# Optimization experiments

Hardware: AMD Instinct MI355X
Metric: run time of the kernel (lower is better)

Reference implementation:

```python
import jax, jax.numpy as jnp
import numpy as np

B, N, F_IN, F_OUT = 64, 4096, 32, 32


def setup_inputs() -> dict:
    key = jax.random.key(0)
    k1, k2, k3, k4 = jax.random.split(key, 4)
    x = jax.random.normal(k1, (B, N, F_IN), dtype=jnp.float32)
    adj = jax.random.uniform(k2, (N, N), dtype=jnp.float32)
    # GraphConvolution parameters (Glorot-ish scale)
    W = jax.random.normal(k3, (F_IN, F_OUT), dtype=jnp.float32) / np.sqrt(F_IN)
    b = jax.random.normal(k4, (F_OUT,), dtype=jnp.float32) * 0.01
    return {"x": x, "adj": adj, "W": W, "b": b}


def reference(x, adj, W, b):
    # Original: adj_ = kron(I_B, adj) -> block-diagonal [B*N, B*N];
    # gconv(x_flat, adj_) = adj_ @ (x_flat @ W) + b, reshaped to [B, N, F_OUT].
    # Block-diagonal structure == independent per-batch graph conv:
    #   out[b] = adj @ (x[b] @ W) + b
    support = jnp.einsum('bnf,fo->bno', x, W)      # [B, N, F_OUT]
    out = jnp.einsum('nm,bmo->bno', adj, support)  # [B, N, F_OUT]
    return out + b
```

## Files before the change

kernel.cpp:

```cpp
#include <hip/hip_runtime.h>
#include <hip/hip_bf16.h>


#define B_SZ 64
#define N_SZ 4096
#define NT 64
#define STG 49152

typedef __attribute__((ext_vector_type(8))) short bf16x8;
typedef __attribute__((ext_vector_type(4))) float f32x4;
typedef __attribute__((ext_vector_type(8))) unsigned short u16x8;

__device__ __forceinline__ unsigned short f2bf(float f) {
  unsigned int u = __float_as_uint(f);
  u += 0x7fffu + ((u >> 16) & 1u);
  return (unsigned short)(u >> 16);
}

__device__ __forceinline__ void support_body(const float* __restrict__ x,
                                             const float* __restrict__ W,
                                             unsigned short* __restrict__ St,
                                             int gid) {
  const int m = gid & (N_SZ - 1);
  const int b = gid >> 12;
  const float4* xr = (const float4*)(x + (size_t)gid * 32);
  float xv[32];
#pragma unroll
  for (int i = 0; i < 8; ++i) {
    float4 v = xr[i];
    xv[4 * i + 0] = v.x; xv[4 * i + 1] = v.y;
    xv[4 * i + 2] = v.z; xv[4 * i + 3] = v.w;
  }
  const size_t obase = ((size_t)b * 32) * (size_t)N_SZ + m;
#pragma unroll
  for (int o = 0; o < 32; ++o) {
    float acc = 0.f;
#pragma unroll
    for (int f = 0; f < 32; ++f) acc = fmaf(xv[f], W[f * 32 + o], acc);
    St[obase + (size_t)o * N_SZ] = f2bf(acc);
  }
}

__device__ __forceinline__ void cvt_body(const float* __restrict__ a,
                                         unsigned short* __restrict__ o,
                                         size_t idx8) {
  const size_t i = idx8 * 8;
  const float4* p = (const float4*)(a + i);
  float4 v0 = p[0], v1 = p[1];
  u16x8 r;
  r[0] = f2bf(v0.x); r[1] = f2bf(v0.y); r[2] = f2bf(v0.z); r[3] = f2bf(v0.w);
  r[4] = f2bf(v1.x); r[5] = f2bf(v1.y); r[6] = f2bf(v1.z); r[7] = f2bf(v1.w);
  *(u16x8*)(o + i) = r;
}

__global__ __launch_bounds__(256) void k_prep(const float* __restrict__ x,
                                              const float* __restrict__ adj,
                                              const float* __restrict__ W,
                                              unsigned short* __restrict__ St,
                                              unsigned short* __restrict__ adjB) {
  const int bid = blockIdx.x;
  const int t = threadIdx.x;
  if (bid < 8192) cvt_body(adj, adjB, (size_t)bid * 256 + t);
  else support_body(x, W, St, (bid - 8192) * 256 + t);
}

__global__ __launch_bounds__(256) void k_support(const float* __restrict__ x,
                                                 const float* __restrict__ W,
                                                 unsigned short* __restrict__ St) {
  support_body(x, W, St, blockIdx.x * 256 + threadIdx.x);
}
__global__ __launch_bounds__(256) void k_cvt(const float* __restrict__ a,
                                             unsigned short* __restrict__ o) {
  cvt_body(a, o, (size_t)blockIdx.x * 256 + threadIdx.x);
}

#define GLOAD16(gp, lp)                                                        \
  __builtin_amdgcn_global_load_lds(                                            \
      (const __attribute__((address_space(1))) void*)(gp),                     \
      (__attribute__((address_space(3))) void*)(lp), 16, 0, 0)
#define PRIO1() __builtin_amdgcn_s_setprio(1)
#define PRIO0() __builtin_amdgcn_s_setprio(0)
#define VMW(N_) asm volatile("s_waitcnt vmcnt(" #N_ ")" ::: "memory")
#define LGKM0() asm volatile("s_waitcnt lgkmcnt(0)" ::: "memory")
#define BARR() asm volatile("s_barrier" ::: "memory")
#define SCHED0() __builtin_amdgcn_sched_barrier(0)

__global__ __launch_bounds__(512, 2) void k_gemm8(const unsigned short* __restrict__ Ab,
                                                  const unsigned short* __restrict__ Bm,
                                                  const float* __restrict__ bias,
                                                  float* __restrict__ out,
                                                  int nbm, int rowoff) {
  __shared__ __attribute__((aligned(16))) char SM[147456];
  const int t = threadIdx.x;
  const int wg = blockIdx.x;
  const int xcd = wg & 7;
  const int c = wg >> 3;
  const int bm0 = (xcd * nbm + (c >> 3)) << 7;
  const int bn0 = (c & 7) << 8;
  const int lane = t & 63;
  const int wid = t >> 6;
  const int wr = wid & 1;
  const int nc = (wid >> 1) & 1;
  const int ks = wid >> 2;

  f32x4 acc[4][8];
#pragma unroll
  for (int i = 0; i < 4; ++i)
#pragma unroll
    for (int j = 0; j < 8; ++j) acc[i][j] = (f32x4){0.f, 0.f, 0.f, 0.f};

  const int srow = t >> 3;
  const int as = t & 7;
  const int swz = (as ^ (srow & 7)) << 4;
  const size_t a_s0 = ((size_t)(bm0 + srow) << 13) + (size_t)swz;
  const size_t b_s0 = ((size_t)(bn0 + srow) << 13) + (size_t)swz;
  const int t16 = t * 16;
  const char* A8 = (const char*)Ab;
  const char* B8 = (const char*)Bm;

#define STAGE(KT_, LOFF_)                                                      \
  do {                                                                         \
    const size_t kb = (size_t)(KT_) << 7;                                      \
    GLOAD16(A8 + a_s0 + kb,           SM + (LOFF_) + t16);                     \
    GLOAD16(A8 + a_s0 + 524288 + kb,  SM + (LOFF_) + 8192 + t16);              \
    GLOAD16(B8 + b_s0 + kb,           SM + (LOFF_) + 16384 + t16);             \
    GLOAD16(B8 + b_s0 + 524288 + kb,  SM + (LOFF_) + 24576 + t16);             \
    GLOAD16(B8 + b_s0 + 1048576 + kb, SM + (LOFF_) + 32768 + t16);             \
    GLOAD16(B8 + b_s0 + 1572864 + kb, SM + (LOFF_) + 40960 + t16);             \
  } while (0)

  const int cbase = (ks * 64 + ((lane >> 4) << 4)) ^ ((lane & 7) << 4);
  int aoff[4], boff[8];
#pragma unroll
  for (int mi = 0; mi < 4; ++mi)
    aoff[mi] = (wr * 64 + mi * 16 + (lane & 15)) * 128 + cbase;
#pragma unroll
  for (int ni = 0; ni < 8; ++ni)
    boff[ni] = 16384 + (nc * 128 + ni * 16 + (lane & 15)) * 128 + cbase;

#define FRAG_MFMA(CUROFF_)                                                     \
  do {                                                                         \
    bf16x8 a[4], b[8];                                                         \
    _Pragma("unroll") for (int mi = 0; mi < 4; ++mi)                           \
        a[mi] = *(const bf16x8*)(SM + (CUROFF_) + aoff[mi]);                   \
    _Pragma("unroll") for (int ni = 0; ni < 8; ++ni)                           \
        b[ni] = *(const bf16x8*)(SM + (CUROFF_) + boff[ni]);                   \
    LGKM0();                                                                   \
    SCHED0();                                                                  \
    BARR();                                                                    \
    PRIO1();                                                                   \
    _Pragma("unroll") for (int mi = 0; mi < 4; ++mi)                           \
        _Pragma("unroll") for (int ni = 0; ni < 8; ++ni)                       \
            acc[mi][ni] = __builtin_amdgcn_mfma_f32_16x16x32_bf16(             \
                a[mi], b[ni], acc[mi][ni], 0, 0, 0);                           \
    PRIO0();                                                                   \
  } while (0)

#define ITER(T_, CUR_, NXT_)                                                   \
  do {                                                                         \
    STAGE((T_) + 2, (NXT_) * STG);                                             \
    VMW(12);                                                                   \
    BARR();                                                                    \
    FRAG_MFMA((CUR_) * STG);                                                   \
  } while (0)

  STAGE(0, 0);
  STAGE(1, STG);

  for (int t0 = 0; t0 < 60; t0 += 3) {
    ITER(t0 + 0, 0, 2);
    ITER(t0 + 1, 1, 0);
    ITER(t0 + 2, 2, 1);
  }
  ITER(60, 0, 2);
  ITER(61, 1, 0);
  VMW(6);
  BARR();
  FRAG_MFMA(2 * STG);
  VMW(0);
  BARR();
  FRAG_MFMA(0 * STG);

  if (ks == 1) {
    char* mb = SM + ((wid & 3) << 15);
#pragma unroll
    for (int mi = 0; mi < 4; ++mi)
#pragma unroll
      for (int ni = 0; ni < 8; ++ni)
        *(f32x4*)(mb + (((mi * 8 + ni) << 6) + lane) * 16) = acc[mi][ni];
  }
  __syncthreads();
  if (ks == 0) {
    char* mb = SM + ((wid & 3) << 15);
#pragma unroll
    for (int mi = 0; mi < 4; ++mi)
#pragma unroll
      for (int ni = 0; ni < 8; ++ni)
        acc[mi][ni] += *(const f32x4*)(mb + (((mi * 8 + ni) << 6) + lane) * 16);
    const float blo = bias[lane & 15];
    const float bhi = bias[(lane & 15) + 16];
#pragma unroll
    for (int mi = 0; mi < 4; ++mi) {
#pragma unroll
      for (int ni = 0; ni < 8; ++ni) {
        const float badd = (ni & 1) ? bhi : blo;
#pragma unroll
        for (int q = 0; q < 4; ++q) {
          const int n = rowoff + bm0 + wr * 64 + mi * 16 + ((lane >> 4) << 2) + q;
          const int cidx = bn0 + nc * 128 + ni * 16 + (lane & 15);
          const int bb = cidx >> 5;
          const int o = cidx & 31;
          out[(((size_t)bb << 12) + n) * 32 + o] = acc[mi][ni][q] + badd;
        }
      }
    }
  }
}

extern "C" void kernel_launch(void* const* d_in, const int* in_sizes, int n_in,
                              void* d_out, int out_size, void* d_ws, size_t ws_size,
                              hipStream_t stream) {
  const float* x = (const float*)d_in[0];
  const float* adj = (const float*)d_in[1];
  const float* W = (const float*)d_in[2];
  const float* bias = (const float*)d_in[3];
  float* out = (float*)d_out;

  const size_t ST_B = (size_t)2048 * 4096 * 2;
  const size_t ADJ_FULL = (size_t)4096 * 4096 * 2;

  unsigned short* St = (unsigned short*)d_ws;

  if (ws_size >= ST_B + ADJ_FULL) {
    unsigned short* adjB = St + (ST_B / 2);
    hipLaunchKernelGGL(k_prep, dim3(9216), dim3(256), 0, stream, x, adj, W, St,
                       adjB);
    hipLaunchKernelGGL(k_gemm8, dim3(256), dim3(512), 0, stream, adjB, St, bias,
                       out, 4, 0);
  } else {
    unsigned short* adjH = St + (ST_B / 2);
    hipLaunchKernelGGL(k_support, dim3((B_SZ * N_SZ) / 256), dim3(256), 0,
                       stream, x, W, St);
    hipLaunchKernelGGL(k_cvt, dim3((2048 * 4096) / 2048), dim3(256), 0, stream,
                       adj, adjH);
    hipLaunchKernelGGL(k_gemm8, dim3(128), dim3(512), 0, stream, adjH, St, bias,
                       out, 2, 0);
    hipLaunchKernelGGL(k_cvt, dim3((2048 * 4096) / 2048), dim3(256), 0, stream,
                       adj + (size_t)2048 * 4096, adjH);
    hipLaunchKernelGGL(k_gemm8, dim3(128), dim3(512), 0, stream, adjH, St, bias,
                       out, 2, 2048);
  }
}
```

Baseline: 96.89 us.

## Interleave global-to-LDS prefetch with MFMA in four sub-phases per k-tile

Restructures the GEMM main loop so each k-tile is split into four phases. Each phase loads two B fragments from LDS, issues part of the next tile's global_load_lds prefetch, then runs eight MFMAs between barriers. This spreads memory issue across the compute instead of issuing all six loads up front with a single wait. It adds several extra s_barriers per tile and disables loop unrolling, which may add synchronisation overhead.

New measurement: 95.96 us. About the same (-1.0%).

```diff
diff --git a/kernel.cpp b/kernel.cpp
--- a/kernel.cpp
+++ b/kernel.cpp
@@ -82,21 +82,21 @@
 #define PRIO0() __builtin_amdgcn_s_setprio(0)
 #define VMW(N_) asm volatile("s_waitcnt vmcnt(" #N_ ")" ::: "memory")
 #define LGKM0() asm volatile("s_waitcnt lgkmcnt(0)" ::: "memory")
-#define BARR() asm volatile("s_barrier" ::: "memory")
+#define BAR() asm volatile("s_barrier" ::: "memory")
 #define SCHED0() __builtin_amdgcn_sched_barrier(0)
 
-__global__ __launch_bounds__(512, 2) void k_gemm8(const unsigned short* __restrict__ Ab,
-                                                  const unsigned short* __restrict__ Bm,
-                                                  const float* __restrict__ bias,
-                                                  float* __restrict__ out,
-                                                  int nbm, int rowoff) {
+__global__ __launch_bounds__(512, 2) void k_gemm8p(const unsigned short* __restrict__ Ab,
+                                                   const unsigned short* __restrict__ Bm,
+                                                   const float* __restrict__ bias,
+                                                   float* __restrict__ out,
+                                                   int nbm, int rowoff) {
   __shared__ __attribute__((aligned(16))) char SM[147456];
   const int t = threadIdx.x;
   const int wg = blockIdx.x;
   const int xcd = wg & 7;
-  const int c = wg >> 3;
-  const int bm0 = (xcd * nbm + (c >> 3)) << 7;
-  const int bn0 = (c & 7) << 8;
+  const int idx = wg >> 3;
+  const int bm0 = (xcd * nbm + (idx >> 3)) << 7;
+  const int bn0 = (idx & 7) << 8;
   const int lane = t & 63;
   const int wid = t >> 6;
   const int wr = wid & 1;
@@ -118,7 +118,16 @@
   const char* A8 = (const char*)Ab;
   const char* B8 = (const char*)Bm;
 
-#define STAGE(KT_, LOFF_)                                                      \
+  const int cbase = (ks * 64 + ((lane >> 4) << 4)) ^ ((lane & 7) << 4);
+  int aoff[4], boff[8];
+#pragma unroll
+  for (int mi = 0; mi < 4; ++mi)
+    aoff[mi] = (wr * 64 + mi * 16 + (lane & 15)) * 128 + cbase;
+#pragma unroll
+  for (int ni = 0; ni < 8; ++ni)
+    boff[ni] = 16384 + (nc * 128 + ni * 16 + (lane & 15)) * 128 + cbase;
+
+#define STAGEALL(KT_, LOFF_)                                                   \
   do {                                                                         \
     const size_t kb = (size_t)(KT_) << 7;                                      \
     GLOAD16(A8 + a_s0 + kb,           SM + (LOFF_) + t16);                     \
@@ -129,57 +138,70 @@
     GLOAD16(B8 + b_s0 + 1572864 + kb, SM + (LOFF_) + 40960 + t16);             \
   } while (0)
 
-  const int cbase = (ks * 64 + ((lane >> 4) << 4)) ^ ((lane & 7) << 4);
-  int aoff[4], boff[8];
-#pragma unroll
-  for (int mi = 0; mi < 4; ++mi)
-    aoff[mi] = (wr * 64 + mi * 16 + (lane & 15)) * 128 + cbase;
-#pragma unroll
-  for (int ni = 0; ni < 8; ++ni)
-    boff[ni] = 16384 + (nc * 128 + ni * 16 + (lane & 15)) * 128 + cbase;
-
-#define FRAG_MFMA(CUROFF_)                                                     \
+#define MFMA2(N0_, N1_)                                                        \
   do {                                                                         \
+    _Pragma("unroll") for (int mi = 0; mi < 4; ++mi) {                         \
+      acc[mi][N0_] = __builtin_amdgcn_mfma_f32_16x16x32_bf16(                  \
+          a[mi], b[N0_], acc[mi][N0_], 0, 0, 0);                               \
+      acc[mi][N1_] = __builtin_amdgcn_mfma_f32_16x16x32_bf16(                  \
+          a[mi], b[N1_], acc[mi][N1_], 0, 0, 0);                               \
+    }                                                                          \
+  } while (0)
+
+#define TILE(T_, CUR_, NXT_, DOST_, VMN_)                                      \
+  do {                                                                         \
+    const char* Lc = SM + (CUR_) * STG;                                        \
+    char* Ln = SM + (NXT_) * STG;                                              \
+    const size_t kb = ((size_t)(T_) + 2) << 7;                                 \
+    (void)Ln; (void)kb;                                                        \
     bf16x8 a[4], b[8];                                                         \
+                                                   \
     _Pragma("unroll") for (int mi = 0; mi < 4; ++mi)                           \
-        a[mi] = *(const bf16x8*)(SM + (CUROFF_) + aoff[mi]);                   \
-    _Pragma("unroll") for (int ni = 0; ni < 8; ++ni)                           \
-        b[ni] = *(const bf16x8*)(SM + (CUROFF_) + boff[ni]);                   \
-    LGKM0();                                                                   \
-    SCHED0();                                                                  \
-    BARR();                                                                    \
-    PRIO1();                                                                   \
-    _Pragma("unroll") for (int mi = 0; mi < 4; ++mi)                           \
-        _Pragma("unroll") for (int ni = 0; ni < 8; ++ni)                       \
-            acc[mi][ni] = __builtin_amdgcn_mfma_f32_16x16x32_bf16(             \
-                a[mi], b[ni], acc[mi][ni], 0, 0, 0);                           \
-    PRIO0();                                                                   \
+        a[mi] = *(const bf16x8*)(Lc + aoff[mi]);                               \
+    b[0] = *(const bf16x8*)(Lc + boff[0]);                                     \
+    b[1] = *(const bf16x8*)(Lc + boff[1]);                                     \
+    if (DOST_) {                                                               \
+      GLOAD16(A8 + a_s0 + kb, Ln + t16);                                       \
+      GLOAD16(A8 + a_s0 + 524288 + kb, Ln + 8192 + t16);                       \
+    }                                                                          \
+    BAR(); LGKM0(); SCHED0(); PRIO1(); MFMA2(0, 1); PRIO0(); BAR();            \
+                                                           \
+    b[2] = *(const bf16x8*)(Lc + boff[2]);                                     \
+    b[3] = *(const bf16x8*)(Lc + boff[3]);                                     \
+    if (DOST_) GLOAD16(B8 + b_s0 + kb, Ln + 16384 + t16);                      \
+    BAR(); LGKM0(); SCHED0(); PRIO1(); MFMA2(2, 3); PRIO0(); BAR();            \
+                                                           \
+    b[4] = *(const bf16x8*)(Lc + boff[4]);                                     \
+    b[5] = *(const bf16x8*)(Lc + boff[5]);                                     \
+    if (DOST_) GLOAD16(B8 + b_s0 + 524288 + kb, Ln + 24576 + t16);             \
+    BAR(); LGKM0(); SCHED0(); PRIO1(); MFMA2(4, 5); PRIO0(); BAR();            \
+                          \
+    b[6] = *(const bf16x8*)(Lc + boff[6]);                                     \
+    b[7] = *(const bf16x8*)(Lc + boff[7]);                                     \
+    if (DOST_) {                                                               \
+      GLOAD16(B8 + b_s0 + 1048576 + kb, Ln + 32768 + t16);                     \
+      GLOAD16(B8 + b_s0 + 1572864 + kb, Ln + 40960 + t16);                     \
+    }                                                                          \
+    BAR(); LGKM0(); SCHED0(); PRIO1(); MFMA2(6, 7); PRIO0();                   \
+    VMN_;                                                                      \
+    BAR();                                                                     \
   } while (0)
 
-#define ITER(T_, CUR_, NXT_)                                                   \
-  do {                                                                         \
-    STAGE((T_) + 2, (NXT_) * STG);                                             \
-    VMW(12);                                                                   \
-    BARR();                                                                    \
-    FRAG_MFMA((CUR_) * STG);                                                   \
-  } while (0)
-
-  STAGE(0, 0);
-  STAGE(1, STG);
-
+  STAGEALL(0, 0);
+  STAGEALL(1, STG);
+  VMW(6);
+  BAR();
+
+#pragma clang loop unroll(disable)
   for (int t0 = 0; t0 < 60; t0 += 3) {
-    ITER(t0 + 0, 0, 2);
-    ITER(t0 + 1, 1, 0);
-    ITER(t0 + 2, 2, 1);
-  }
-  ITER(60, 0, 2);
-  ITER(61, 1, 0);
-  VMW(6);
-  BARR();
-  FRAG_MFMA(2 * STG);
-  VMW(0);
-  BARR();
-  FRAG_MFMA(0 * STG);
+    TILE(t0 + 0, 0, 2, 1, VMW(6));
+    TILE(t0 + 1, 1, 0, 1, VMW(6));
+    TILE(t0 + 2, 2, 1, 1, VMW(6));
+  }
+  TILE(60, 0, 2, 1, VMW(6));
+  TILE(61, 1, 0, 1, VMW(6));
+  TILE(62, 2, 1, 0, VMW(0));
+  TILE(63, 0, 1, 0, );
 
   if (ks == 1) {
     char* mb = SM + ((wid & 3) << 15);
@@ -235,19 +257,19 @@
     unsigned short* adjB = St + (ST_B / 2);
     hipLaunchKernelGGL(k_prep, dim3(9216), dim3(256), 0, stream, x, adj, W, St,
                        adjB);
-    hipLaunchKernelGGL(k_gemm8, dim3(256), dim3(512), 0, stream, adjB, St, bias,
-                       out, 4, 0);
+    hipLaunchKernelGGL(k_gemm8p, dim3(256), dim3(512), 0, stream, adjB, St,
+                       bias, out, 4, 0);
   } else {
     unsigned short* adjH = St + (ST_B / 2);
     hipLaunchKernelGGL(k_support, dim3((B_SZ * N_SZ) / 256), dim3(256), 0,
                        stream, x, W, St);
     hipLaunchKernelGGL(k_cvt, dim3((2048 * 4096) / 2048), dim3(256), 0, stream,
                        adj, adjH);
-    hipLaunchKernelGGL(k_gemm8, dim3(128), dim3(512), 0, stream, adjH, St, bias,
-                       out, 2, 0);
+    hipLaunchKernelGGL(k_gemm8p, dim3(128), dim3(512), 0, stream, adjH, St,
+                       bias, out, 2, 0);
     hipLaunchKernelGGL(k_cvt, dim3((2048 * 4096) / 2048), dim3(256), 0, stream,
                        adj + (size_t)2048 * 4096, adjH);
-    hipLaunchKernelGGL(k_gemm8, dim3(128), dim3(512), 0, stream, adjH, St, bias,
-                       out, 2, 2048);
-  }
-}
+    hipLaunchKernelGGL(k_gemm8p, dim3(128), dim3(512), 0, stream, adjH, St,
+                       bias, out, 2, 2048);
+  }
+}
```
